# Performance work log

Measured on AMD Instinct MI355X. Metric: run time of the kernel, lower is better.

## Reference

```python
import jax, jax.numpy as jnp
import numpy as np

N_EMBD = 1024
N_HEAD = 16
HEAD = N_EMBD // N_HEAD


def setup_inputs() -> dict:
    key = jax.random.key(0)
    k1, k2, k3 = jax.random.split(key, 3)
    x = jax.random.normal(k1, (2, 2048, N_EMBD), dtype=jnp.float32)
    # torch Linear weight is [out, in]; store transposed for x @ W
    W_attn = jax.random.normal(k2, (N_EMBD, 3 * N_EMBD), dtype=jnp.float32) * (1.0 / np.sqrt(N_EMBD))
    W_proj = jax.random.normal(k3, (N_EMBD, N_EMBD), dtype=jnp.float32) * (1.0 / np.sqrt(N_EMBD))
    return {"x": x, "W_attn": W_attn, "W_proj": W_proj}


def reference(x, W_attn, W_proj):
    B, T, C = x.shape
    qkv = x @ W_attn  # [B,T,3C]
    q, k, v = jnp.split(qkv, 3, axis=-1)
    # [B,T,H,D] -> [B,H,T,D]
    q = q.reshape(B, T, N_HEAD, HEAD).transpose(0, 2, 1, 3)
    k = k.reshape(B, T, N_HEAD, HEAD).transpose(0, 2, 1, 3)
    v = v.reshape(B, T, N_HEAD, HEAD).transpose(0, 2, 1, 3)
    att = jnp.einsum('bhqd,bhkd->bhqk', q, k) * (1.0 / np.sqrt(HEAD))
    causal = jnp.tril(jnp.ones((T, T), dtype=bool))
    att = jnp.where(causal[None, None], att, jnp.float32(-jnp.inf))
    att = jax.nn.softmax(att, axis=-1)
    y = jnp.einsum('bhqk,bhkd->bhqd', att, v)
    y = y.transpose(0, 2, 1, 3).reshape(B, T, C)
    return y @ W_proj
```

## Files before the change

kernel.cpp:

```cpp
#include <hip/hip_runtime.h>

typedef unsigned short u16;
typedef __bf16 bf16x8 __attribute__((ext_vector_type(8)));
typedef float f32x4 __attribute__((ext_vector_type(4)));

#define BB 2
#define TT 2048
#define CC 1024
#define HH 16
#define DD 64
#define MM (BB*TT)

__device__ __forceinline__ u16 f2b(float f) {
    union { float f; unsigned int i; } a; a.f = f;
    unsigned int u = a.i;
    unsigned int r = (u + 0x7FFFu + ((u >> 16) & 1u)) >> 16;
    return (u16)r;
}
__device__ __forceinline__ u16 f2b_fast(float f) {
    union { float f; unsigned int i; } a; a.f = f;
    return (u16)((a.i + 0x8000u) >> 16);
}

__device__ __forceinline__ void gld16(const u16* g, u16* l) {
    __builtin_amdgcn_global_load_lds(
        (const __attribute__((address_space(1))) unsigned int*)g,
        (__attribute__((address_space(3))) unsigned int*)l, 16, 0, 0);
}

__global__ __launch_bounds__(256) void prep_k(const float* __restrict__ x,
                                              u16* __restrict__ xb,
                                              const float* __restrict__ Wa,
                                              u16* __restrict__ Wat,
                                              const float* __restrict__ Wp,
                                              u16* __restrict__ Wpt) {
    __shared__ u16 tile[64][65];
    const int b = blockIdx.x;
    const int tid = threadIdx.x;
    if (b < 4096) {
        int i = b * 256 + tid;
        float4 v = ((const float4*)x)[i];
        ushort4 o;
        o.x = f2b(v.x); o.y = f2b(v.y); o.z = f2b(v.z); o.w = f2b(v.w);
        ((ushort4*)xb)[i] = o;
        return;
    }
    const float* in; u16* out; int K, N, n0, k0;
    if (b < 4096 + 768) {
        int bb = b - 4096;
        in = Wa; out = Wat; K = 1024; N = 3072;
        n0 = (bb % 48) * 64; k0 = (bb / 48) * 64;
    } else {
        int bb = b - 4096 - 768;
        in = Wp; out = Wpt; K = 1024; N = 1024;
        n0 = (bb % 16) * 64; k0 = (bb / 16) * 64;
    }
    const int tx = tid & 63, ty = tid >> 6;
    for (int i = 0; i < 16; i++) {
        int row = ty + i * 4;
        tile[row][tx] = f2b(in[(size_t)(k0 + row) * N + n0 + tx]);
    }
    __syncthreads();
    for (int i = 0; i < 16; i++) {
        int row = ty + i * 4;
        out[(size_t)(n0 + row) * K + k0 + tx] = tile[tx][row];
    }
}

__global__ __launch_bounds__(256) void transpose_v_k(const u16* __restrict__ in,
                                                     u16* __restrict__ out) {
    __shared__ u16 tile[64][65];
    int t0 = blockIdx.x * 64, bh = blockIdx.y;
    const u16* src = in + (size_t)bh * TT * DD;
    u16* dst = out + (size_t)bh * DD * TT;
    int tx = threadIdx.x, ty = threadIdx.y;
    for (int i = 0; i < 16; i++) {
        int row = ty + i * 4;
        tile[row][tx] = src[(size_t)(t0 + row) * DD + tx];
    }
    __syncthreads();
    for (int i = 0; i < 16; i++) {
        int row = ty + i * 4;
        dst[(size_t)row * TT + t0 + tx] = tile[tx][row];
    }
}

template<int MODE>
__global__ __launch_bounds__(256) void gemm_k(const u16* __restrict__ A,
                                              const u16* __restrict__ Bt,
                                              u16* __restrict__ Cq,
                                              u16* __restrict__ Ck,
                                              u16* __restrict__ Cv,
                                              float* __restrict__ Cout,
                                              int N, int K) {
    __shared__ __attribute__((aligned(16))) u16 As[2][128 * 32];
    __shared__ __attribute__((aligned(16))) u16 Bs[2][128 * 32];
    const int tid  = threadIdx.x;
    const int lane = tid & 63, w = tid >> 6;
    const int wm = w >> 1, wn = w & 1;
    const int quad = lane >> 4, l16 = lane & 15;

    const int nwg = gridDim.x, lin = blockIdx.x;
    const int cpx = nwg >> 3;
    const int sw  = (lin & 7) * cpx + (lin >> 3);
    const int ncols = N >> 7;
    const int m0 = (sw / ncols) * 128, n0 = (sw % ncols) * 128;

    f32x4 acc[4][4];
    for (int mi = 0; mi < 4; mi++)
        for (int ni = 0; ni < 4; ni++)
            for (int e = 0; e < 4; e++) acc[mi][ni][e] = 0.f;

#define GSTAGE(BUF, K0)                                                   \
    for (int i = 0; i < 2; i++) {                                         \
        int c = tid + 256 * i;                                            \
        int row = c >> 2, col = (c & 3) * 8;                              \
        const u16* srcA;                                                  \
        if constexpr (MODE == 0) {                                        \
            srcA = A + (size_t)(m0 + row) * K + (K0) + col;               \
        } else {                                                          \
            int m = m0 + row;                                             \
            int b = m >> 11, t = m & 2047;                                \
            int kk = (K0) + col;                                          \
            int h = kk >> 6, d = kk & 63;                                 \
            srcA = A + ((size_t)(b * HH + h) * TT + t) * DD + d;          \
        }                                                                 \
        gld16(srcA, &As[BUF][c * 8]);                                     \
        gld16(Bt + (size_t)(n0 + row) * K + (K0) + col, &Bs[BUF][c * 8]); \
    }

    GSTAGE(0, 0);
    const int nk = K >> 5;
    for (int jk = 0; jk < nk; jk++) {
        const int cb = jk & 1;
        __syncthreads();
        if (jk + 1 < nk) { GSTAGE(cb ^ 1, (jk + 1) * 32); }
        bf16x8 af[4], bfm[4];
        for (int mi = 0; mi < 4; mi++)
            af[mi] = *(const bf16x8*)&As[cb][(wm * 64 + mi * 16 + l16) * 32 + quad * 8];
        for (int ni = 0; ni < 4; ni++)
            bfm[ni] = *(const bf16x8*)&Bs[cb][(wn * 64 + ni * 16 + l16) * 32 + quad * 8];
        for (int mi = 0; mi < 4; mi++)
            for (int ni = 0; ni < 4; ni++)
                acc[mi][ni] = __builtin_amdgcn_mfma_f32_16x16x32_bf16(
                    af[mi], bfm[ni], acc[mi][ni], 0, 0, 0);
    }
#undef GSTAGE

    const float SCQ = 0.125f * 1.44269504f;
    for (int mi = 0; mi < 4; mi++)
        for (int ni = 0; ni < 4; ni++)
            for (int r = 0; r < 4; r++) {
                int row = m0 + wm * 64 + mi * 16 + quad * 4 + r;
                int col = n0 + wn * 64 + ni * 16 + l16;
                if constexpr (MODE == 0) {
                    int which = col >> 10;
                    int h = (col >> 6) & 15, d = col & 63;
                    int b = row >> 11, t = row & 2047;
                    size_t off = ((size_t)(b * HH + h) * TT + t) * DD + d;
                    float val = acc[mi][ni][r];
                    if (which == 0) val *= SCQ;
                    (which == 0 ? Cq : which == 1 ? Ck : Cv)[off] = f2b(val);
                } else {
                    Cout[(size_t)row * N + col] = acc[mi][ni][r];
                }
            }
}

__global__ __launch_bounds__(256, 2) void attn_k(const u16* __restrict__ Q,
                                                 const u16* __restrict__ Kb,
                                                 const u16* __restrict__ Vtg,
                                                 u16* __restrict__ Y) {
    __shared__ __attribute__((aligned(16))) u16 Ks[2][128 * 64];
    __shared__ __attribute__((aligned(16))) u16 Vs[2][64 * 128];
    __shared__ __attribute__((aligned(16))) u16 Ps[4][16 * 128];
    const int tid  = threadIdx.x;
    const int lane = tid & 63, w = tid >> 6;
    const int quad = lane >> 4, l16 = lane & 15;
    const int bh = blockIdx.x;
    const int y  = blockIdx.y;
    const int rowi = (y >> 1) & 3, coli = y >> 3;
    const int basew = ((coli & 1) ? 9 : 16) - ((coli >> 1) << 3);
    const int work = basew + ((coli & 1) ? rowi : -rowi);
    const int sb = 2 * (work - 1) + (y & 1);
    const int nkt = work;
    const size_t base  = (size_t)bh * TT * DD;
    const size_t baseV = (size_t)bh * DD * TT;

    int ksidx[4], koff[4], voff[4];
    for (int r = 0; r < 4; r++) {
        int sidx = r * 256 + tid;
        ksidx[r] = sidx;
        int kr = sidx >> 3, ksl = sidx & 7;
        koff[r] = kr * 64 + ((ksl ^ (kr & 7)) << 3);
        int vr = sidx >> 4, vsl = sidx & 15;
        voff[r] = vr * TT + ((vsl ^ (vr & 7)) << 3);
    }
    const u16* kg = Kb + base;
    const u16* vg = Vtg + baseV;

    for (int r = 0; r < 4; r++) gld16(kg + koff[r], &Ks[0][ksidx[r] * 8]);
    for (int r = 0; r < 4; r++) gld16(vg + voff[r], &Vs[0][ksidx[r] * 8]);

    bf16x8 qf[2];
    for (int kk = 0; kk < 2; kk++)
        qf[kk] = *(const bf16x8*)(Q + base +
            (size_t)(sb * 64 + w * 16 + l16) * DD + kk * 32 + quad * 8);

    const int swx = (l16 & 7);
    const int swk0 = ((quad ^ swx) << 3);
    const int swk1 = (((4 + quad) ^ swx) << 3);

    float mst[4], lst[4];
    f32x4 oacc[4];
    for (int r = 0; r < 4; r++) { mst[r] = -1e30f; lst[r] = 0.f; }
    for (int nd = 0; nd < 4; nd++)
        for (int e = 0; e < 4; e++) oacc[nd][e] = 0.f;

    for (int jk = 0; jk < nkt; jk++) {
        const int cb = jk & 1;
        __syncthreads();

        if (jk + 1 < nkt) {
            const u16* kn = kg + (size_t)(jk + 1) * (128 * DD);
            const u16* vn = vg + (size_t)(jk + 1) * 128;
            for (int r = 0; r < 4; r++)
                gld16(kn + koff[r], &Ks[cb ^ 1][ksidx[r] * 8]);
            for (int r = 0; r < 4; r++)
                gld16(vn + voff[r], &Vs[cb ^ 1][ksidx[r] * 8]);
        }

        f32x4 s[8];
        for (int ni = 0; ni < 8; ni++)
            for (int e = 0; e < 4; e++) s[ni][e] = 0.f;
        {
            bf16x8 kfa[8];
            for (int ni = 0; ni < 8; ni++)
                kfa[ni] = *(const bf16x8*)&Ks[cb][(ni * 16 + l16) * 64 + swk0];
            for (int ni = 0; ni < 8; ni++)
                s[ni] = __builtin_amdgcn_mfma_f32_16x16x32_bf16(
                    qf[0], kfa[ni], s[ni], 0, 0, 0);
        }
        {
            bf16x8 kfa[8];
            for (int ni = 0; ni < 8; ni++)
                kfa[ni] = *(const bf16x8*)&Ks[cb][(ni * 16 + l16) * 64 + swk1];
            for (int ni = 0; ni < 8; ni++)
                s[ni] = __builtin_amdgcn_mfma_f32_16x16x32_bf16(
                    qf[1], kfa[ni], s[ni], 0, 0, 0);
        }

        if (jk == (sb >> 1)) {
            int row0 = sb * 64 + w * 16 + quad * 4;
            int col0 = jk * 128 + l16;
            for (int ni = 0; ni < 8; ni++)
                for (int r = 0; r < 4; r++)
                    if (col0 + ni * 16 > row0 + r) s[ni][r] = -1e30f;
        }
        float alpha[4];
        for (int r = 0; r < 4; r++) {
            float mx = s[0][r];
            for (int ni = 1; ni < 8; ni++) mx = fmaxf(mx, s[ni][r]);
            for (int off = 8; off >= 1; off >>= 1)
                mx = fmaxf(mx, __shfl_xor(mx, off));
            float mn = fmaxf(mst[r], mx);
            alpha[r] = __builtin_amdgcn_exp2f(mst[r] - mn);
            mst[r] = mn;
        }
        float rs[4] = {0.f, 0.f, 0.f, 0.f};
        for (int ni = 0; ni < 8; ni++)
            for (int r = 0; r < 4; r++) {
                float pv = __builtin_amdgcn_exp2f(s[ni][r] - mst[r]);
                rs[r] += pv;
                int row = quad * 4 + r;
                int cg  = ni * 2 + (l16 >> 3);
                Ps[w][row * 128 + ((cg ^ row) << 3) + (l16 & 7)] = f2b_fast(pv);
            }
        for (int r = 0; r < 4; r++) {
            float sm = rs[r];
            for (int off = 8; off >= 1; off >>= 1)
                sm += __shfl_xor(sm, off);
            lst[r] = lst[r] * alpha[r] + sm;
            for (int nd = 0; nd < 4; nd++) oacc[nd][r] *= alpha[r];
        }

        for (int kk = 0; kk < 4; kk++) {
            const int swv = (((kk * 4 + quad) ^ swx) << 3);
            bf16x8 vfa[4];
            for (int nd = 0; nd < 4; nd++)
                vfa[nd] = *(const bf16x8*)&Vs[cb][(nd * 16 + l16) * 128 + swv];
            bf16x8 pf = *(const bf16x8*)&Ps[w][l16 * 128 +
                (((kk * 4 + quad) ^ l16) << 3)];
            for (int nd = 0; nd < 4; nd++)
                oacc[nd] = __builtin_amdgcn_mfma_f32_16x16x32_bf16(
                    pf, vfa[nd], oacc[nd], 0, 0, 0);
        }
    }

    for (int nd = 0; nd < 4; nd++)
        for (int r = 0; r < 4; r++) {
            int row = sb * 64 + w * 16 + quad * 4 + r;
            int col = nd * 16 + l16;
            Y[base + (size_t)row * DD + col] = f2b(oacc[nd][r] / lst[r]);
        }
}

extern "C" void kernel_launch(void* const* d_in, const int* in_sizes, int n_in,
                              void* d_out, int out_size, void* d_ws, size_t ws_size,
                              hipStream_t stream) {
    const float* x      = (const float*)d_in[0];
    const float* W_attn = (const float*)d_in[1];
    const float* W_proj = (const float*)d_in[2];
    float* out = (float*)d_out;

    u16* Wt_attn = (u16*)d_ws;
    u16* Wt_proj = Wt_attn + 3072 * 1024;
    u16* xb      = Wt_proj + 1024 * 1024;
    u16* q       = xb + (size_t)MM * CC;
    u16* k       = q + (size_t)32 * 2048 * 64;
    u16* v       = k + (size_t)32 * 2048 * 64;
    u16* y       = v + (size_t)32 * 2048 * 64;
    u16* vt      = xb;

    prep_k<<<dim3(4096 + 768 + 256), 256, 0, stream>>>(
        x, xb, W_attn, Wt_attn, W_proj, Wt_proj);
    gemm_k<0><<<dim3((MM / 128) * (3072 / 128)), 256, 0, stream>>>(
        xb, Wt_attn, q, k, v, nullptr, 3072, 1024);
    transpose_v_k<<<dim3(TT / 64, BB * HH), dim3(64, 4), 0, stream>>>(v, vt);
    attn_k<<<dim3(32, 32), 256, 0, stream>>>(q, k, vt, y);
    gemm_k<1><<<dim3((MM / 128) * (1024 / 128)), 256, 0, stream>>>(
        y, Wt_proj, nullptr, nullptr, nullptr, out, 1024, 1024);
}
```

Before: 194.1 us.

## Fuse V transpose into QKV GEMM epilogue and narrow projection GEMM tile

The QKV GEMM epilogue now writes V tiles already transposed to [b,h,d,t] by staging them through a padded LDS buffer and issuing 16-byte stores, so the separate transpose_v_k kernel and its extra round trip through global memory go away. The output projection GEMM moves to a 128x64 tile, which doubles its block count so the GPU's compute units are better filled. The costs are a larger LDS footprint in MODE 0, extra barriers in the V-tile epilogue, and less data reuse per block in the projection GEMM.

```diff
diff --git a/kernel.cpp b/kernel.cpp
--- a/kernel.cpp
+++ b/kernel.cpp
@@ -67,24 +67,6 @@
     }
 }
 
-__global__ __launch_bounds__(256) void transpose_v_k(const u16* __restrict__ in,
-                                                     u16* __restrict__ out) {
-    __shared__ u16 tile[64][65];
-    int t0 = blockIdx.x * 64, bh = blockIdx.y;
-    const u16* src = in + (size_t)bh * TT * DD;
-    u16* dst = out + (size_t)bh * DD * TT;
-    int tx = threadIdx.x, ty = threadIdx.y;
-    for (int i = 0; i < 16; i++) {
-        int row = ty + i * 4;
-        tile[row][tx] = src[(size_t)(t0 + row) * DD + tx];
-    }
-    __syncthreads();
-    for (int i = 0; i < 16; i++) {
-        int row = ty + i * 4;
-        dst[(size_t)row * TT + t0 + tx] = tile[tx][row];
-    }
-}
-
 template<int MODE>
 __global__ __launch_bounds__(256) void gemm_k(const u16* __restrict__ A,
                                               const u16* __restrict__ Bt,
@@ -93,8 +75,14 @@
                                               u16* __restrict__ Cv,
                                               float* __restrict__ Cout,
                                               int N, int K) {
-    __shared__ __attribute__((aligned(16))) u16 As[2][128 * 32];
-    __shared__ __attribute__((aligned(16))) u16 Bs[2][128 * 32];
+    constexpr int BN   = (MODE == 0) ? 128 : 64;
+    constexpr int NF   = (MODE == 0) ? 4 : 2;
+    constexpr int BSU  = BN * 32;
+    constexpr int LDSZ = (MODE == 0) ? (128 * 136) : (2 * 4096 + 2 * BSU);
+    __shared__ __attribute__((aligned(16))) u16 smem[LDSZ];
+#define AsP(B) (smem + (B) * 4096)
+#define BsP(B) (smem + 8192 + (B) * BSU)
+
     const int tid  = threadIdx.x;
     const int lane = tid & 63, w = tid >> 6;
     const int wm = w >> 1, wn = w & 1;
@@ -103,31 +91,41 @@
     const int nwg = gridDim.x, lin = blockIdx.x;
     const int cpx = nwg >> 3;
     const int sw  = (lin & 7) * cpx + (lin >> 3);
-    const int ncols = N >> 7;
-    const int m0 = (sw / ncols) * 128, n0 = (sw % ncols) * 128;
-
-    f32x4 acc[4][4];
+    const int ncols = N / BN;
+    const int m0 = (sw / ncols) * 128, n0 = (sw % ncols) * BN;
+
+    f32x4 acc[4][NF];
     for (int mi = 0; mi < 4; mi++)
-        for (int ni = 0; ni < 4; ni++)
+        for (int ni = 0; ni < NF; ni++)
             for (int e = 0; e < 4; e++) acc[mi][ni][e] = 0.f;
 
-#define GSTAGE(BUF, K0)                                                   \
-    for (int i = 0; i < 2; i++) {                                         \
-        int c = tid + 256 * i;                                            \
-        int row = c >> 2, col = (c & 3) * 8;                              \
-        const u16* srcA;                                                  \
-        if constexpr (MODE == 0) {                                        \
-            srcA = A + (size_t)(m0 + row) * K + (K0) + col;               \
-        } else {                                                          \
-            int m = m0 + row;                                             \
-            int b = m >> 11, t = m & 2047;                                \
-            int kk = (K0) + col;                                          \
-            int h = kk >> 6, d = kk & 63;                                 \
-            srcA = A + ((size_t)(b * HH + h) * TT + t) * DD + d;          \
-        }                                                                 \
-        gld16(srcA, &As[BUF][c * 8]);                                     \
-        gld16(Bt + (size_t)(n0 + row) * K + (K0) + col, &Bs[BUF][c * 8]); \
-    }
+#define GSTAGE(BUF, K0) do {                                                  \
+    for (int i = 0; i < 2; i++) {                                             \
+        int c = tid + 256 * i;                                                \
+        int row = c >> 2, col = (c & 3) * 8;                                  \
+        const u16* srcA;                                                      \
+        if constexpr (MODE == 0) {                                            \
+            srcA = A + (size_t)(m0 + row) * K + (K0) + col;                   \
+        } else {                                                              \
+            int m = m0 + row;                                                 \
+            int b = m >> 11, t = m & 2047;                                    \
+            int kk = (K0) + col;                                              \
+            int h = kk >> 6, d = kk & 63;                                     \
+            srcA = A + ((size_t)(b * HH + h) * TT + t) * DD + d;              \
+        }                                                                     \
+        gld16(srcA, AsP(BUF) + c * 8);                                        \
+    }                                                                         \
+    if constexpr (MODE == 0) {                                                \
+        for (int i = 0; i < 2; i++) {                                         \
+            int c = tid + 256 * i;                                            \
+            int row = c >> 2, col = (c & 3) * 8;                              \
+            gld16(Bt + (size_t)(n0 + row) * K + (K0) + col, BsP(BUF) + c * 8);\
+        }                                                                     \
+    } else {                                                                  \
+        int row = tid >> 2, col = (tid & 3) * 8;                              \
+        gld16(Bt + (size_t)(n0 + row) * K + (K0) + col, BsP(BUF) + tid * 8);  \
+    }                                                                         \
+} while (0)
 
     GSTAGE(0, 0);
     const int nk = K >> 5;
@@ -135,36 +133,65 @@
         const int cb = jk & 1;
         __syncthreads();
         if (jk + 1 < nk) { GSTAGE(cb ^ 1, (jk + 1) * 32); }
-        bf16x8 af[4], bfm[4];
+        bf16x8 af[4], bfm[NF];
         for (int mi = 0; mi < 4; mi++)
-            af[mi] = *(const bf16x8*)&As[cb][(wm * 64 + mi * 16 + l16) * 32 + quad * 8];
-        for (int ni = 0; ni < 4; ni++)
-            bfm[ni] = *(const bf16x8*)&Bs[cb][(wn * 64 + ni * 16 + l16) * 32 + quad * 8];
+            af[mi] = *(const bf16x8*)(AsP(cb) + (wm * 64 + mi * 16 + l16) * 32 + quad * 8);
+        for (int ni = 0; ni < NF; ni++)
+            bfm[ni] = *(const bf16x8*)(BsP(cb) + ((BN / 2) * wn + ni * 16 + l16) * 32 + quad * 8);
         for (int mi = 0; mi < 4; mi++)
-            for (int ni = 0; ni < 4; ni++)
+            for (int ni = 0; ni < NF; ni++)
                 acc[mi][ni] = __builtin_amdgcn_mfma_f32_16x16x32_bf16(
                     af[mi], bfm[ni], acc[mi][ni], 0, 0, 0);
     }
 #undef GSTAGE
 
-    const float SCQ = 0.125f * 1.44269504f;
-    for (int mi = 0; mi < 4; mi++)
-        for (int ni = 0; ni < 4; ni++)
-            for (int r = 0; r < 4; r++) {
-                int row = m0 + wm * 64 + mi * 16 + quad * 4 + r;
-                int col = n0 + wn * 64 + ni * 16 + l16;
-                if constexpr (MODE == 0) {
-                    int which = col >> 10;
-                    int h = (col >> 6) & 15, d = col & 63;
-                    int b = row >> 11, t = row & 2047;
-                    size_t off = ((size_t)(b * HH + h) * TT + t) * DD + d;
-                    float val = acc[mi][ni][r];
-                    if (which == 0) val *= SCQ;
-                    (which == 0 ? Cq : which == 1 ? Ck : Cv)[off] = f2b(val);
-                } else {
+    if constexpr (MODE == 0) {
+        const float SCQ = 0.125f * 1.44269504f;
+        const int which = n0 >> 10;
+        if (which < 2) {
+            for (int mi = 0; mi < 4; mi++)
+                for (int ni = 0; ni < 4; ni++)
+                    for (int r = 0; r < 4; r++) {
+                        int row = m0 + wm * 64 + mi * 16 + quad * 4 + r;
+                        int col = n0 + wn * 64 + ni * 16 + l16;
+                        int h = (col >> 6) & 15, d = col & 63;
+                        int b = row >> 11, t = row & 2047;
+                        size_t off = ((size_t)(b * HH + h) * TT + t) * DD + d;
+                        float val = acc[mi][ni][r];
+                        if (which == 0) val *= SCQ;
+                        (which == 0 ? Cq : Ck)[off] = f2b(val);
+                    }
+        } else {
+            __syncthreads();
+            for (int mi = 0; mi < 4; mi++)
+                for (int ni = 0; ni < 4; ni++)
+                    for (int r = 0; r < 4; r++) {
+                        int cl = wn * 64 + ni * 16 + l16;
+                        int tl = wm * 64 + mi * 16 + quad * 4 + r;
+                        smem[cl * 136 + tl] = f2b(acc[mi][ni][r]);
+                    }
+            __syncthreads();
+            const int b = m0 >> 11, t0l = m0 & 2047;
+            const int c0 = n0 - 2048;
+            for (int j = 0; j < 8; j++) {
+                int idx = j * 256 + tid;
+                int cl = idx >> 4, ch = idx & 15;
+                int cg = c0 + cl, h = cg >> 6, d = cg & 63;
+                uint4 val = *(const uint4*)&smem[cl * 136 + ch * 8];
+                *(uint4*)&Cv[((size_t)(b * HH + h) * DD + d) * TT + t0l + ch * 8] = val;
+            }
+        }
+    } else {
+        for (int mi = 0; mi < 4; mi++)
+            for (int ni = 0; ni < NF; ni++)
+                for (int r = 0; r < 4; r++) {
+                    int row = m0 + wm * 64 + mi * 16 + quad * 4 + r;
+                    int col = n0 + wn * 32 + ni * 16 + l16;
                     Cout[(size_t)row * N + col] = acc[mi][ni][r];
                 }
-            }
+    }
+#undef AsP
+#undef BsP
 }
 
 __global__ __launch_bounds__(256, 2) void attn_k(const u16* __restrict__ Q,
@@ -318,16 +345,14 @@
     u16* xb      = Wt_proj + 1024 * 1024;
     u16* q       = xb + (size_t)MM * CC;
     u16* k       = q + (size_t)32 * 2048 * 64;
-    u16* v       = k + (size_t)32 * 2048 * 64;
-    u16* y       = v + (size_t)32 * 2048 * 64;
-    u16* vt      = xb;
+    u16* vt      = k + (size_t)32 * 2048 * 64;
+    u16* y       = vt + (size_t)32 * 2048 * 64;
 
     prep_k<<<dim3(4096 + 768 + 256), 256, 0, stream>>>(
         x, xb, W_attn, Wt_attn, W_proj, Wt_proj);
     gemm_k<0><<<dim3((MM / 128) * (3072 / 128)), 256, 0, stream>>>(
-        xb, Wt_attn, q, k, v, nullptr, 3072, 1024);
-    transpose_v_k<<<dim3(TT / 64, BB * HH), dim3(64, 4), 0, stream>>>(v, vt);
+        xb, Wt_attn, q, k, vt, nullptr, 3072, 1024);
     attn_k<<<dim3(32, 32), 256, 0, stream>>>(q, k, vt, y);
-    gemm_k<1><<<dim3((MM / 128) * (1024 / 128)), 256, 0, stream>>>(
+    gemm_k<1><<<dim3((MM / 128) * (1024 / 64)), 256, 0, stream>>>(
         y, Wt_proj, nullptr, nullptr, nullptr, out, 1024, 1024);
 }
```

Result: faster. 181.1 us (-6.7%).
